# Kernel tuning notes

Measured on AMD Instinct MI355X. Metric: run time of the kernel, lower is better.

## Reference

```python
import jax, jax.numpy as jnp
import numpy as np

EMB_DIM = 1024
NUM_HEADS = 16
HEAD_DIM = EMB_DIM // NUM_HEADS  # 64
B, S = 2, 2048


def setup_inputs() -> dict:
    key = jax.random.key(0)
    ks = jax.random.split(key, 9)
    scale = 1.0 / np.sqrt(EMB_DIM)
    return {
        "query": jax.random.normal(ks[0], (B, S, EMB_DIM), dtype=jnp.float32),
        "Wq": jax.random.normal(ks[1], (EMB_DIM, EMB_DIM), dtype=jnp.float32) * scale,
        "bq": jax.random.normal(ks[2], (EMB_DIM,), dtype=jnp.float32) * 0.01,
        "Wk": jax.random.normal(ks[3], (EMB_DIM, EMB_DIM), dtype=jnp.float32) * scale,
        "bk": jax.random.normal(ks[4], (EMB_DIM,), dtype=jnp.float32) * 0.01,
        "Wv": jax.random.normal(ks[5], (EMB_DIM, EMB_DIM), dtype=jnp.float32) * scale,
        "bv": jax.random.normal(ks[6], (EMB_DIM,), dtype=jnp.float32) * 0.01,
        "Wo": jax.random.normal(ks[7], (EMB_DIM, EMB_DIM), dtype=jnp.float32) * scale,
        "bo": jax.random.normal(ks[8], (EMB_DIM,), dtype=jnp.float32) * 0.01,
    }


def reference(query, Wq, bq, Wk, bk, Wv, bv, Wo, bo):
    # Self-attention path (key_value=None, mask=None in the original forward).
    b, s, _ = query.shape
    # torch nn.Linear: y = x @ W.T + b
    def proj(x, W, bias):
        y = jnp.einsum('bse,fe->bsf', x, W) + bias
        # [B,S,E] -> [B,H,S,D]
        return y.reshape(b, s, NUM_HEADS, HEAD_DIM).transpose(0, 2, 1, 3)

    q = proj(query, Wq, bq)
    k = proj(query, Wk, bk)
    v = proj(query, Wv, bv)

    scores = jnp.einsum('bhqd,bhkd->bhqk', q, k) / np.sqrt(HEAD_DIM).astype(np.float32)
    attn = jax.nn.softmax(scores, axis=-1)  # [B,H,S,S]
    out = jnp.einsum('bhqk,bhkd->bhqd', attn, v)
    out = out.transpose(0, 2, 1, 3).reshape(b, s, EMB_DIM)
    return jnp.einsum('bse,fe->bsf', out, Wo) + bo
```

## Files before the change

kernel.cpp:

```cpp
#include <hip/hip_runtime.h>
#include <hip/hip_bf16.h>

using bf16x4 = __attribute__((ext_vector_type(4))) short;
using short8 = __attribute__((ext_vector_type(8))) short;
using f32x4  = __attribute__((ext_vector_type(4))) float;
using u32x2  = __attribute__((ext_vector_type(2))) unsigned;

__device__ __forceinline__ short f2bf(float f) {
  unsigned u = __builtin_bit_cast(unsigned, f);
  u = (u + 0x7fffu + ((u >> 16) & 1u)) >> 16;
  return (short)u;
}
__device__ __forceinline__ unsigned pk2(float a, float b) {
  __hip_bfloat162 h = __float22bfloat162_rn(make_float2(a, b));
  unsigned u; __builtin_memcpy(&u, &h, 4);
  return u;
}
__device__ __forceinline__ void gload16(const short* g, short* l) {
  __builtin_amdgcn_global_load_lds(
      (const __attribute__((address_space(1))) unsigned int*)g,
      (__attribute__((address_space(3))) unsigned int*)l, 16, 0, 0);
}

constexpr int E  = 1024;
constexpr int SL = 2048;
constexpr int NB = 2;
constexpr int NH = 16;
constexpr int M  = NB * SL;

__global__ __launch_bounds__(256) void convert_kernel(
    const float* __restrict__ X,  const float* __restrict__ Wq,
    const float* __restrict__ Wk, const float* __restrict__ Wv,
    const float* __restrict__ Wo, short* __restrict__ out)
{
  const size_t i8 = ((size_t)blockIdx.x * 256 + threadIdx.x) * 8;
  const float* src;
  if (i8 < (size_t)(4u << 20)) {
    src = X + i8;
  } else {
    size_t r = i8 - (size_t)(4u << 20);
    int wi = (int)(r >> 20);
    size_t off = r & ((1u << 20) - 1);
    src = (wi == 0 ? Wq : wi == 1 ? Wk : wi == 2 ? Wv : Wo) + off;
  }
  f32x4 a = *(const f32x4*)src;
  f32x4 b = *(const f32x4*)(src + 4);
  short hb[8];
#pragma unroll
  for (int e = 0; e < 4; ++e) { hb[e] = f2bf(a[e]); hb[4 + e] = f2bf(b[e]); }
  *(short8*)(out + i8) = *(short8*)hb;
}

template <int TM, int TN, bool OUTF32, bool FUSEV>
__global__ __launch_bounds__(256) void gemm_kernel(
    const short* __restrict__ A0, const short* __restrict__ A1, const short* __restrict__ A2,
    const short* __restrict__ W0, const short* __restrict__ W1, const short* __restrict__ W2,
    const float* __restrict__ b0, const float* __restrict__ b1, const float* __restrict__ b2,
    void* __restrict__ Y0, void* __restrict__ Y1, void* __restrict__ Y2,
    float s0, float s1, float s2, int ld0, int ld1, int ld2)
{
  constexpr int BK = 32;
  constexpr int RA = TM / 64;
  constexpr int RB = TN / 64;
  constexpr int WM = TM / 2, WN = TN / 2;
  constexpr int NI = WM / 16, NJ = WN / 16;
  __shared__ alignas(16) short As[2][TM * BK];
  __shared__ alignas(16) short Bs[2][TN * BK];
  const int t = threadIdx.x;
  const int l = t & 63;
  const int w = t >> 6;
  const int c = l & 15;
  const int g = l >> 4;
  const int z = blockIdx.z;
  const short* Ap = (z == 0) ? A0 : (z == 1) ? A1 : A2;
  const short* Wp = (z == 0) ? W0 : (z == 1) ? W1 : W2;
  const float* bp = (z == 0) ? b0 : (z == 1) ? b1 : b2;
  void* Yp        = (z == 0) ? Y0 : (z == 1) ? Y1 : Y2;
  const float sc  = (z == 0) ? s0 : (z == 1) ? s1 : s2;
  const int ldY   = (z == 0) ? ld0 : (z == 1) ? ld1 : ld2;
  const bool vtr  = FUSEV && (z == 2);
  const int m0 = (vtr ? blockIdx.y : blockIdx.x) * TM;
  const int n0 = (vtr ? blockIdx.x : blockIdx.y) * TN;

  const short* gA[RA]; int oA[RA];
  const short* gB[RB]; int oB[RB];
#pragma unroll
  for (int r = 0; r < RA; ++r) {
    const int cc = r * 256 + t;
    gA[r] = Ap + (size_t)(m0 + (cc >> 2)) * E + (cc & 3) * 8;
    oA[r] = (r * 256 + (t & ~63)) * 8;
  }
#pragma unroll
  for (int r = 0; r < RB; ++r) {
    const int cc = r * 256 + t;
    gB[r] = Wp + (size_t)(n0 + (cc >> 2)) * E + (cc & 3) * 8;
    oB[r] = (r * 256 + (t & ~63)) * 8;
  }

#pragma unroll
  for (int r = 0; r < RA; ++r) gload16(gA[r], &As[0][oA[r]]);
#pragma unroll
  for (int r = 0; r < RB; ++r) gload16(gB[r], &Bs[0][oB[r]]);

  const int wm = (w >> 1) * WM;
  const int wn = (w & 1) * WN;
  f32x4 acc[NI][NJ] = {};
  int cur = 0;

  for (int k0 = 0; k0 < E; k0 += BK) {
    __syncthreads();
    if (k0 + BK < E) {
#pragma unroll
      for (int r = 0; r < RA; ++r) gload16(gA[r] + k0 + BK, &As[cur ^ 1][oA[r]]);
#pragma unroll
      for (int r = 0; r < RB; ++r) gload16(gB[r] + k0 + BK, &Bs[cur ^ 1][oB[r]]);
    }
    short8 ah[NI], bfr[NJ];
#pragma unroll
    for (int i = 0; i < NI; ++i)
      ah[i] = *(const short8*)&As[cur][(wm + i * 16 + c) * BK + g * 8];
#pragma unroll
    for (int j = 0; j < NJ; ++j)
      bfr[j] = *(const short8*)&Bs[cur][(wn + j * 16 + c) * BK + g * 8];
#pragma unroll
    for (int i = 0; i < NI; ++i)
#pragma unroll
      for (int j = 0; j < NJ; ++j)
        acc[i][j] = __builtin_amdgcn_mfma_f32_16x16x32_bf16(ah[i], bfr[j], acc[i][j], 0, 0, 0);
    cur ^= 1;
  }

#pragma unroll
  for (int j = 0; j < NJ; ++j) {
    const int col = n0 + wn + j * 16 + c;
    const float bcol = vtr ? 0.f : bp[col];
#pragma unroll
    for (int i = 0; i < NI; ++i) {
      const int rowb = m0 + wm + i * 16 + g * 4;
#pragma unroll
      for (int r = 0; r < 4; ++r) {
        const int row = rowb + r;
        const float bias = vtr ? bp[row] : bcol;
        const float v = (acc[i][j][r] + bias) * sc;
        if (OUTF32) ((float*)Yp)[(size_t)row * ldY + col] = v;
        else        ((short*)Yp)[(size_t)row * ldY + col] = f2bf(v);
      }
    }
  }
}

__global__ __launch_bounds__(512) void flash_kernel(
    const short* __restrict__ Qm, const short* __restrict__ Km,
    const short* __restrict__ VTm, short* __restrict__ Oh)
{
  __shared__ alignas(16) short Ks[64][72];
  __shared__ alignas(16) short Vt[64][72];
  __shared__ alignas(16) short Pl[8][16][72];
  const int t = threadIdx.x;
  const int l = t & 63;
  const int w = t >> 6;
  const int c = l & 15;
  const int g = l >> 4;
  const int q0 = blockIdx.x * 128;
  const int bh = (int)blockIdx.y;
  const int b = bh >> 4;
  const int h = bh & 15;
  const size_t baseK = (size_t)b * SL * E + h * 64;
  const size_t baseV = (size_t)(h * 64) * M + (size_t)b * SL;

  short8 aq[2];
  {
    const short* qp = Qm + baseK + (size_t)(q0 + w * 16 + c) * E + g * 8;
    aq[0] = *(const short8*)qp;
    aq[1] = *(const short8*)(qp + 32);
  }

  f32x4 lacc = {0.f, 0.f, 0.f, 0.f};
  f32x4 acc_o[4] = {};

  const int srow = t >> 3, sseg = t & 7;
  const short* gK = Km + baseK + (size_t)srow * E + sseg * 8;
  const short* gV = VTm + baseV + (size_t)srow * M + sseg * 8;

  short8 kreg = *(const short8*)gK;
  short8 vreg = *(const short8*)gV;

  constexpr int NT = SL / 64;
  for (int kt = 0; kt < NT; ++kt) {
    __syncthreads();
    *(short8*)&Ks[srow][sseg * 8] = kreg;
    *(short8*)&Vt[srow][sseg * 8] = vreg;
    __syncthreads();
    if (kt + 1 < NT) {
      kreg = *(const short8*)(gK + (size_t)(kt + 1) * 64 * E);
      vreg = *(const short8*)(gV + (kt + 1) * 64);
    }

    f32x4 st[4] = {};
#pragma unroll
    for (int j = 0; j < 4; ++j)
#pragma unroll
      for (int kc = 0; kc < 2; ++kc) {
        short8 kf = *(const short8*)&Ks[j * 16 + c][kc * 32 + g * 8];
        st[j] = __builtin_amdgcn_mfma_f32_16x16x32_bf16(kf, aq[kc], st[j], 0, 0, 0);
      }

#pragma unroll
    for (int j = 0; j < 4; ++j) {
      f32x4 p;
#pragma unroll
      for (int r = 0; r < 4; ++r) p[r] = __builtin_amdgcn_exp2f(st[j][r]);
      lacc += p;
      u32x2 pk = {pk2(p[0], p[1]), pk2(p[2], p[3])};
      *(u32x2*)&Pl[w][c][j * 16 + g * 4] = pk;
    }
    short8 ap[2];
    ap[0] = *(const short8*)&Pl[w][c][g * 8];
    ap[1] = *(const short8*)&Pl[w][c][32 + g * 8];

#pragma unroll
    for (int j = 0; j < 4; ++j)
#pragma unroll
      for (int kc = 0; kc < 2; ++kc) {
        short8 vf = *(const short8*)&Vt[j * 16 + c][kc * 32 + g * 8];
        acc_o[j] = __builtin_amdgcn_mfma_f32_16x16x32_bf16(vf, ap[kc], acc_o[j], 0, 0, 0);
      }
  }

  float s = lacc[0] + lacc[1] + lacc[2] + lacc[3];
  s += __shfl_xor(s, 16);
  s += __shfl_xor(s, 32);
  const float inv = 1.0f / s;

  const int token = q0 + w * 16 + c;
  const size_t obase = ((size_t)b * SL + token) * E + h * 64;
#pragma unroll
  for (int j = 0; j < 4; ++j) {
    u32x2 o2 = {pk2(acc_o[j][0] * inv, acc_o[j][1] * inv),
                pk2(acc_o[j][2] * inv, acc_o[j][3] * inv)};
    *(u32x2*)(Oh + obase + j * 16 + g * 4) = o2;
  }
}

extern "C" void kernel_launch(void* const* d_in, const int* in_sizes, int n_in,
                              void* d_out, int out_size, void* d_ws, size_t ws_size,
                              hipStream_t stream)
{
  const float* X  = (const float*)d_in[0];
  const float* Wq = (const float*)d_in[1];
  const float* bq = (const float*)d_in[2];
  const float* Wk = (const float*)d_in[3];
  const float* bk = (const float*)d_in[4];
  const float* Wv = (const float*)d_in[5];
  const float* bv = (const float*)d_in[6];
  const float* Wo = (const float*)d_in[7];
  const float* bo = (const float*)d_in[8];
  float* out = (float*)d_out;

  const size_t szX = (size_t)M * E;
  const size_t szW = (size_t)E * E;
  short* Xb  = (short*)d_ws;
  short* Wqb = Xb + szX;
  short* Wkb = Wqb + szW;
  short* Wvb = Wkb + szW;
  short* Wob = Wvb + szW;
  short* Qw  = Wob + szW;
  short* Kw  = Qw + szX;
  short* VTw = Kw + szX;

  convert_kernel<<<4096, 256, 0, stream>>>(X, Wq, Wk, Wv, Wo, Xb);

  const float kLog2eOver8 = 0.18033688011112042f;
  dim3 g1(M / 128, E / 128, 3);
  gemm_kernel<128, 128, false, true><<<g1, 256, 0, stream>>>(
      Xb, Xb, Wvb,
      Wqb, Wkb, Xb,
      bq, bk, bv,
      (void*)Qw, (void*)Kw, (void*)VTw,
      kLog2eOver8, 1.0f, 1.0f, E, E, M);

  dim3 g2(SL / 128, NB * NH);
  flash_kernel<<<g2, 512, 0, stream>>>(Qw, Kw, VTw, Qw );

  dim3 g3(M / 128, E / 64, 1);
  gemm_kernel<128, 64, true, false><<<g3, 256, 0, stream>>>(
      Qw, Qw, Qw,
      Wob, Wob, Wob,
      bo, bo, bo,
      (void*)out, (void*)out, (void*)out,
      1.0f, 1.0f, 1.0f, E, E, E);
}
```

Measured before the change: 210.4 us.

## Double-buffer K/V tiles and give each flash wave two query sub-tiles

The flash kernel now runs 256 threads per block, and each wave handles 32 query rows (two 16-row sub-tiles), so every K/V fragment read from LDS feeds twice as many MFMAs. K/V tiles are double-buffered in LDS, with the next tile stored and the one after prefetched into registers, which drops one barrier per iteration. The cost is more registers per thread (two accumulator sets, plus K and V fragments held in registers) and fewer waves per block, which may reduce occupancy and latency hiding.

```diff
diff --git a/kernel.cpp b/kernel.cpp
--- a/kernel.cpp
+++ b/kernel.cpp
@@ -149,13 +149,13 @@
   }
 }
 
-__global__ __launch_bounds__(512) void flash_kernel(
+__global__ __launch_bounds__(256) void flash_kernel(
     const short* __restrict__ Qm, const short* __restrict__ Km,
     const short* __restrict__ VTm, short* __restrict__ Oh)
 {
-  __shared__ alignas(16) short Ks[64][72];
-  __shared__ alignas(16) short Vt[64][72];
-  __shared__ alignas(16) short Pl[8][16][72];
+  __shared__ alignas(16) short Ks[2][64][72];
+  __shared__ alignas(16) short Vt[2][64][72];
+  __shared__ alignas(16) short Pl[4][32][72];
   const int t = threadIdx.x;
   const int l = t & 63;
   const int w = t >> 6;
@@ -164,81 +164,122 @@
   const int q0 = blockIdx.x * 128;
   const int bh = (int)blockIdx.y;
   const int b = bh >> 4;
-  const int h = bh & 15;
-  const size_t baseK = (size_t)b * SL * E + h * 64;
-  const size_t baseV = (size_t)(h * 64) * M + (size_t)b * SL;
-
-  short8 aq[2];
-  {
-    const short* qp = Qm + baseK + (size_t)(q0 + w * 16 + c) * E + g * 8;
-    aq[0] = *(const short8*)qp;
-    aq[1] = *(const short8*)(qp + 32);
-  }
-
-  f32x4 lacc = {0.f, 0.f, 0.f, 0.f};
-  f32x4 acc_o[4] = {};
-
-  const int srow = t >> 3, sseg = t & 7;
-  const short* gK = Km + baseK + (size_t)srow * E + sseg * 8;
-  const short* gV = VTm + baseV + (size_t)srow * M + sseg * 8;
-
-  short8 kreg = *(const short8*)gK;
-  short8 vreg = *(const short8*)gV;
+  const int hh = bh & 15;
+  const size_t baseK = (size_t)b * SL * E + hh * 64;
+  const size_t baseV = (size_t)(hh * 64) * M + (size_t)b * SL;
+
+  short8 aq[2][2];
+#pragma unroll
+  for (int u = 0; u < 2; ++u) {
+    const short* qp = Qm + baseK + (size_t)(q0 + w * 32 + u * 16 + c) * E + g * 8;
+    aq[u][0] = *(const short8*)qp;
+    aq[u][1] = *(const short8*)(qp + 32);
+  }
+
+  f32x4 lacc[2] = {{0.f,0.f,0.f,0.f},{0.f,0.f,0.f,0.f}};
+  f32x4 acc_o[2][4] = {};
+
+  const int r0 = t >> 3, s0 = t & 7;
+  const short* gK0 = Km + baseK + (size_t)r0 * E + s0 * 8;
+  const short* gK1 = gK0 + (size_t)32 * E;
+  const short* gV0 = VTm + baseV + (size_t)r0 * M + s0 * 8;
+  const short* gV1 = gV0 + (size_t)32 * M;
+
+  short8 k0r = *(const short8*)gK0, k1r = *(const short8*)gK1;
+  short8 v0r = *(const short8*)gV0, v1r = *(const short8*)gV1;
+  *(short8*)&Ks[0][r0][s0 * 8]      = k0r;
+  *(short8*)&Ks[0][r0 + 32][s0 * 8] = k1r;
+  *(short8*)&Vt[0][r0][s0 * 8]      = v0r;
+  *(short8*)&Vt[0][r0 + 32][s0 * 8] = v1r;
+  k0r = *(const short8*)(gK0 + (size_t)64 * E);
+  k1r = *(const short8*)(gK1 + (size_t)64 * E);
+  v0r = *(const short8*)(gV0 + 64);
+  v1r = *(const short8*)(gV1 + 64);
+  __syncthreads();
 
   constexpr int NT = SL / 64;
+  int cur = 0;
   for (int kt = 0; kt < NT; ++kt) {
+    if (kt + 1 < NT) {
+      *(short8*)&Ks[cur ^ 1][r0][s0 * 8]      = k0r;
+      *(short8*)&Ks[cur ^ 1][r0 + 32][s0 * 8] = k1r;
+      *(short8*)&Vt[cur ^ 1][r0][s0 * 8]      = v0r;
+      *(short8*)&Vt[cur ^ 1][r0 + 32][s0 * 8] = v1r;
+      if (kt + 2 < NT) {
+        k0r = *(const short8*)(gK0 + (size_t)(kt + 2) * 64 * E);
+        k1r = *(const short8*)(gK1 + (size_t)(kt + 2) * 64 * E);
+        v0r = *(const short8*)(gV0 + (kt + 2) * 64);
+        v1r = *(const short8*)(gV1 + (kt + 2) * 64);
+      }
+    }
+
+    short8 kf[4][2];
+#pragma unroll
+    for (int j = 0; j < 4; ++j)
+#pragma unroll
+      for (int kc = 0; kc < 2; ++kc)
+        kf[j][kc] = *(const short8*)&Ks[cur][j * 16 + c][kc * 32 + g * 8];
+
+    f32x4 st[2][4] = {};
+#pragma unroll
+    for (int u = 0; u < 2; ++u)
+#pragma unroll
+      for (int j = 0; j < 4; ++j)
+#pragma unroll
+        for (int kc = 0; kc < 2; ++kc)
+          st[u][j] = __builtin_amdgcn_mfma_f32_16x16x32_bf16(kf[j][kc], aq[u][kc], st[u][j], 0, 0, 0);
+
+#pragma unroll
+    for (int u = 0; u < 2; ++u)
+#pragma unroll
+      for (int j = 0; j < 4; ++j) {
+        f32x4 p;
+#pragma unroll
+        for (int r = 0; r < 4; ++r) p[r] = __builtin_amdgcn_exp2f(st[u][j][r]);
+        lacc[u] += p;
+        u32x2 pk = {pk2(p[0], p[1]), pk2(p[2], p[3])};
+        *(u32x2*)&Pl[w][u * 16 + c][j * 16 + g * 4] = pk;
+      }
+
+    short8 ap[2][2];
+#pragma unroll
+    for (int u = 0; u < 2; ++u) {
+      ap[u][0] = *(const short8*)&Pl[w][u * 16 + c][g * 8];
+      ap[u][1] = *(const short8*)&Pl[w][u * 16 + c][32 + g * 8];
+    }
+    short8 vf[4][2];
+#pragma unroll
+    for (int j = 0; j < 4; ++j)
+#pragma unroll
+      for (int kc = 0; kc < 2; ++kc)
+        vf[j][kc] = *(const short8*)&Vt[cur][j * 16 + c][kc * 32 + g * 8];
+
+#pragma unroll
+    for (int u = 0; u < 2; ++u)
+#pragma unroll
+      for (int j = 0; j < 4; ++j)
+#pragma unroll
+        for (int kc = 0; kc < 2; ++kc)
+          acc_o[u][j] = __builtin_amdgcn_mfma_f32_16x16x32_bf16(vf[j][kc], ap[u][kc], acc_o[u][j], 0, 0, 0);
+
     __syncthreads();
-    *(short8*)&Ks[srow][sseg * 8] = kreg;
-    *(short8*)&Vt[srow][sseg * 8] = vreg;
-    __syncthreads();
-    if (kt + 1 < NT) {
-      kreg = *(const short8*)(gK + (size_t)(kt + 1) * 64 * E);
-      vreg = *(const short8*)(gV + (kt + 1) * 64);
-    }
-
-    f32x4 st[4] = {};
-#pragma unroll
-    for (int j = 0; j < 4; ++j)
-#pragma unroll
-      for (int kc = 0; kc < 2; ++kc) {
-        short8 kf = *(const short8*)&Ks[j * 16 + c][kc * 32 + g * 8];
-        st[j] = __builtin_amdgcn_mfma_f32_16x16x32_bf16(kf, aq[kc], st[j], 0, 0, 0);
-      }
-
+    cur ^= 1;
+  }
+
+#pragma unroll
+  for (int u = 0; u < 2; ++u) {
+    float s = lacc[u][0] + lacc[u][1] + lacc[u][2] + lacc[u][3];
+    s += __shfl_xor(s, 16);
+    s += __shfl_xor(s, 32);
+    const float inv = 1.0f / s;
+    const int token = q0 + w * 32 + u * 16 + c;
+    const size_t obase = ((size_t)b * SL + token) * E + hh * 64;
 #pragma unroll
     for (int j = 0; j < 4; ++j) {
-      f32x4 p;
-#pragma unroll
-      for (int r = 0; r < 4; ++r) p[r] = __builtin_amdgcn_exp2f(st[j][r]);
-      lacc += p;
-      u32x2 pk = {pk2(p[0], p[1]), pk2(p[2], p[3])};
-      *(u32x2*)&Pl[w][c][j * 16 + g * 4] = pk;
-    }
-    short8 ap[2];
-    ap[0] = *(const short8*)&Pl[w][c][g * 8];
-    ap[1] = *(const short8*)&Pl[w][c][32 + g * 8];
-
-#pragma unroll
-    for (int j = 0; j < 4; ++j)
-#pragma unroll
-      for (int kc = 0; kc < 2; ++kc) {
-        short8 vf = *(const short8*)&Vt[j * 16 + c][kc * 32 + g * 8];
-        acc_o[j] = __builtin_amdgcn_mfma_f32_16x16x32_bf16(vf, ap[kc], acc_o[j], 0, 0, 0);
-      }
-  }
-
-  float s = lacc[0] + lacc[1] + lacc[2] + lacc[3];
-  s += __shfl_xor(s, 16);
-  s += __shfl_xor(s, 32);
-  const float inv = 1.0f / s;
-
-  const int token = q0 + w * 16 + c;
-  const size_t obase = ((size_t)b * SL + token) * E + h * 64;
-#pragma unroll
-  for (int j = 0; j < 4; ++j) {
-    u32x2 o2 = {pk2(acc_o[j][0] * inv, acc_o[j][1] * inv),
-                pk2(acc_o[j][2] * inv, acc_o[j][3] * inv)};
-    *(u32x2*)(Oh + obase + j * 16 + g * 4) = o2;
+      u32x2 o2 = {pk2(acc_o[u][j][0] * inv, acc_o[u][j][1] * inv),
+                  pk2(acc_o[u][j][2] * inv, acc_o[u][j][3] * inv)};
+      *(u32x2*)(Oh + obase + j * 16 + g * 4) = o2;
+    }
   }
 }
 
@@ -280,7 +321,7 @@
       kLog2eOver8, 1.0f, 1.0f, E, E, M);
 
   dim3 g2(SL / 128, NB * NH);
-  flash_kernel<<<g2, 512, 0, stream>>>(Qw, Kw, VTw, Qw );
+  flash_kernel<<<g2, 256, 0, stream>>>(Qw, Kw, VTw, Qw );
 
   dim3 g3(M / 128, E / 64, 1);
   gemm_kernel<128, 64, true, false><<<g3, 256, 0, stream>>>(
```

Result: no change. 213.9 us (+1.7%).
